# Optimization experiments

Measured on AMD Instinct MI355X. Metric: run time of the kernel, lower is better.

## Reference

```python
import jax, jax.numpy as jnp
import numpy as np

H, W = 32, 32
DIM = 768
NUM_BLOCKS = 4
BLOCK = DIM // NUM_BLOCKS
SCALE = 0.02


def setup_inputs() -> dict:
    key = jax.random.key(0)
    k0, k1, k2, k3, k4 = jax.random.split(key, 5)
    B, N, C = 64, H * W, DIM
    x = jax.random.normal(k0, (B, N, C), dtype=jnp.float32)
    w1 = SCALE * jax.random.normal(k1, (2, NUM_BLOCKS, BLOCK, BLOCK), dtype=jnp.float32)
    b1 = SCALE * jax.random.normal(k2, (2, NUM_BLOCKS, BLOCK), dtype=jnp.float32)
    w2 = SCALE * jax.random.normal(k3, (2, NUM_BLOCKS, BLOCK, BLOCK), dtype=jnp.float32)
    b2 = SCALE * jax.random.normal(k4, (2, NUM_BLOCKS, BLOCK), dtype=jnp.float32)
    return {"x": x, "w1": w1, "b1": b1, "w2": w2, "b2": b2}


def _mul(inp, weights):
    # inp: [B, H, Wf, blocks, d], weights: [blocks, d, k]
    return jnp.einsum('...bd,bdk->...bk', inp, weights)


def reference(x, w1, b1, w2, b2):
    B, N, C = x.shape
    xg = x.reshape(B, H, W, C)
    xf = jnp.fft.rfft2(xg, axes=(1, 2), norm='ortho')  # [B, H, W//2+1, C] complex64
    xf = xf.reshape(B, xf.shape[1], xf.shape[2], NUM_BLOCKS, BLOCK)
    xr, xi = xf.real, xf.imag
    # layer 1: complex block-diagonal linear + ReLU
    r1 = jax.nn.relu(_mul(xr, w1[0]) - _mul(xi, w1[1]) + b1[0])
    i1 = jax.nn.relu(_mul(xr, w1[1]) + _mul(xi, w1[0]) + b1[1])
    # layer 2 (faithful to original: imag uses the already-updated real part)
    r2 = _mul(r1, w2[0]) - _mul(i1, w2[1]) + b2[0]
    i2 = _mul(r2, w2[1]) + _mul(i1, w2[0]) + b2[1]
    xc = (r2 + 1j * i2).reshape(B, r2.shape[1], r2.shape[2], C)
    out = jnp.fft.irfft2(xc, s=(H, W), axes=(1, 2), norm='ortho')
    return out.reshape(B, N, C) + jnp.zeros_like(x)  # bias is zeros (self.bias is None)
```

## Files before the change

kernel.cpp:

```cpp
#include <hip/hip_runtime.h>
#include <cstddef>
#include <cstdint>


typedef __attribute__((ext_vector_type(8))) short bf16x8;
typedef __attribute__((ext_vector_type(4))) float f32x4;

namespace {

constexpr int BATCH = 64;
constexpr int WF    = 17;
constexpr int CC    = 768;
constexpr int BLK   = 192;

constexpr size_t W_ELEMS  = 24u * 36864u;
constexpr size_t TW_ELEMS = 8u * 1024u;
constexpr size_t PW_ELEMS = W_ELEMS + TW_ELEMS;

constexpr int PLANE_U = 48 * 512;

constexpr float C32[32] = {
   1.0000000000f,  0.9807852804f,  0.9238795325f,  0.8314696123f,
   0.7071067812f,  0.5555702330f,  0.3826834324f,  0.1950903220f,
   0.0000000000f, -0.1950903220f, -0.3826834324f, -0.5555702330f,
  -0.7071067812f, -0.8314696123f, -0.9238795325f, -0.9807852804f,
  -1.0000000000f, -0.9807852804f, -0.9238795325f, -0.8314696123f,
  -0.7071067812f, -0.5555702330f, -0.3826834324f, -0.1950903220f,
   0.0000000000f,  0.1950903220f,  0.3826834324f,  0.5555702330f,
   0.7071067812f,  0.8314696123f,  0.9238795325f,  0.9807852804f
};
constexpr float S32[32] = {
   0.0000000000f,  0.1950903220f,  0.3826834324f,  0.5555702330f,
   0.7071067812f,  0.8314696123f,  0.9238795325f,  0.9807852804f,
   1.0000000000f,  0.9807852804f,  0.9238795325f,  0.8314696123f,
   0.7071067812f,  0.5555702330f,  0.3826834324f,  0.1950903220f,
   0.0000000000f, -0.1950903220f, -0.3826834324f, -0.5555702330f,
  -0.7071067812f, -0.8314696123f, -0.9238795325f, -0.9807852804f,
  -1.0000000000f, -0.9807852804f, -0.9238795325f, -0.8314696123f,
  -0.7071067812f, -0.5555702330f, -0.3826834324f, -0.1950903220f
};

}

__device__ __forceinline__ ushort f2bf(float f) {
    union { float f; unsigned u; } v; v.f = f;
    const unsigned r = (v.u + 0x7FFFu + ((v.u >> 16) & 1u)) >> 16;
    return (ushort)r;
}
__device__ __forceinline__ uint pk(float lo, float hi) {
    return (uint)f2bf(lo) | ((uint)f2bf(hi) << 16);
}

__global__ __launch_bounds__(256) void k_pack(const float* __restrict__ w1,
                                              const float* __restrict__ w2,
                                              ushort* __restrict__ pw) {
    const unsigned idx = blockIdx.x * 256u + threadIdx.x;
    if (idx < W_ELEMS) {
        const unsigned mi = idx / 36864u;
        const unsigned r  = idx % 36864u;
        const unsigned kk = r / 6144u;
        const unsigned r2 = r % 6144u;
        const unsigned nf = r2 / 512u;
        const unsigned r3 = r2 % 512u;
        const unsigned lane = r3 / 8u;
        const unsigned i  = r3 % 8u;
        const unsigned d   = kk * 32u + (lane >> 4) * 8u + i;
        const unsigned col = nf * 16u + (lane & 15u);
        const unsigned mat = mi >> 2, blk = mi & 3u;
        const float* src; float sgn = 1.f;
        if      (mat == 0u) src = w1 + (size_t)(0 * 4 + blk) * BLK * BLK;
        else if (mat == 1u) src = w1 + (size_t)(1 * 4 + blk) * BLK * BLK;
        else if (mat == 2u) { src = w1 + (size_t)(1 * 4 + blk) * BLK * BLK; sgn = -1.f; }
        else if (mat == 3u) src = w2 + (size_t)(0 * 4 + blk) * BLK * BLK;
        else if (mat == 4u) src = w2 + (size_t)(1 * 4 + blk) * BLK * BLK;
        else                { src = w2 + (size_t)(1 * 4 + blk) * BLK * BLK; sgn = -1.f; }
        pw[idx] = f2bf(sgn * src[(size_t)d * BLK + col]);
    } else if (idx < PW_ELEMS) {
        const unsigned t = idx - (unsigned)W_ELEMS;
        const unsigned mat = t >> 10;
        const unsigned rr  = t & 1023u;
        const unsigned mf  = rr >> 9;
        const unsigned q   = rr & 511u;
        const unsigned lane = q >> 3, i = q & 7u;
        const unsigned row = mf * 16u + (lane & 15u);
        const unsigned col = (lane >> 4) * 8u + i;
        const unsigned ang = (row * col) & 31u;
        float v;
        if      (mat == 0u) v = C32[ang] * 0.03125f;
        else if (mat == 1u) v = S32[ang] * 0.03125f;
        else if (mat == 2u) v = -S32[ang] * 0.03125f;
        else if (mat == 3u) v = C32[ang];
        else if (mat == 4u) v = S32[ang];
        else if (mat == 5u) v = -S32[ang];
        else if (mat == 6u) {
            if      (col == 0u)  v = 0.03125f;
            else if (col < 16u)  v = 2.f * C32[ang] * 0.03125f;
            else if (col == 16u) v = C32[(16u * row) & 31u] * 0.03125f;
            else                 v = 0.f;
        } else {
            v = (col >= 1u && col <= 15u) ? (-2.f * S32[ang] * 0.03125f) : 0.f;
        }
        pw[idx] = f2bf(v);
    }
}

__global__ __launch_bounds__(256) void k_rfft_w(const float* __restrict__ x,
                                                ushort* __restrict__ spec,
                                                const ushort* __restrict__ pw) {
    __shared__ uint xb[16 * 384];

    const int bid = blockIdx.x;
    const int cq = bid & 3;
    const int hp = (bid >> 2) & 15;
    const int b  = bid >> 6;
    const int tid = threadIdx.x;
    const int wv = tid >> 6, l = tid & 63, lc = l & 15, lg = l >> 4;

#pragma unroll
    for (int it = 0; it < 6; ++it) {
        const int flat = it * 256 + tid;
        const int h  = flat / 768;
        const int rm = flat % 768;
        const int wp = rm / 48;
        const int c4 = rm % 48;
        const float* p = x + ((size_t)(b * 1024 + (hp * 2 + h) * 32 + wp * 2) * CC)
                           + cq * 192 + c4 * 4;
        const float4 a  = *(const float4*)p;
        const float4 bb = *(const float4*)(p + CC);
        uint4 u;
        u.x = pk(a.x, bb.x); u.y = pk(a.y, bb.y);
        u.z = pk(a.z, bb.z); u.w = pk(a.w, bb.w);
        const int col = (h * 192 + c4 * 4) ^ (((wp >> 2) & 3) << 3);
        *(uint4*)&xb[wp * 384 + col] = u;
    }
    __syncthreads();

    const ushort* TW = pw + W_ELEMS;
    bf16x8 ac[2], as[2];
#pragma unroll
    for (int m = 0; m < 2; ++m) {
        ac[m] = *(const bf16x8*)(TW + ((size_t)(3 * 2 + m) * 64 + l) * 8);
        as[m] = *(const bf16x8*)(TW + ((size_t)(5 * 2 + m) * 64 + l) * 8);
    }

    f32x4 aR[2][6] = {}, aI[2][6] = {};
#pragma unroll
    for (int j = 0; j < 6; ++j) {
        const int nf = (j < 3) ? (wv * 3 + j) : (12 + wv * 3 + (j - 3));
        union { bf16x8 v; uint d[4]; } u;
#pragma unroll
        for (int t = 0; t < 4; ++t) {
            const int wp = lg * 4 + t;
            u.d[t] = xb[wp * 384 + ((nf * 16 + lc) ^ (lg << 3))];
        }
#pragma unroll
        for (int m = 0; m < 2; ++m) {
            aR[m][j] = __builtin_amdgcn_mfma_f32_16x16x32_bf16(ac[m], u.v, aR[m][j], 0, 0, 0);
            aI[m][j] = __builtin_amdgcn_mfma_f32_16x16x32_bf16(as[m], u.v, aI[m][j], 0, 0, 0);
        }
    }

    uint* spec32 = (uint*)spec;
    const int swz = (hp & 7) << 1;
#pragma unroll
    for (int m = 0; m < 2; ++m)
#pragma unroll
        for (int j = 0; j < 3; ++j)
#pragma unroll
            for (int r = 0; r < 4; ++r) {
                if (m == 1 && (lg != 0 || r != 0)) continue;
                const int kw = m * 16 + lg * 4 + r;
                const int csub = cq * 12 + wv * 3 + j;
                const size_t pos = ((size_t)(b * WF + kw) * 2) * 12288
                                 + csub * 256 + hp * 16 + (lc ^ swz);
                spec32[pos]         = pk(aR[m][j][r], aR[m][j + 3][r]);
                spec32[pos + 12288] = pk(aI[m][j][r], aI[m][j + 3][r]);
            }
}

__global__ __launch_bounds__(256, 3) void k_fft_mix(
        ushort* __restrict__ spec,
        const ushort* __restrict__ pw,
        const float* __restrict__ b1, const float* __restrict__ b2) {

    __shared__ ushort lds[4][6336];

    const int bid = blockIdx.x;
    const int blk = bid / (BATCH * WF);
    const int rem = bid % (BATCH * WF);
    const int b   = rem / WF;
    const int kw  = rem % WF;
    const int tid = threadIdx.x;
    const int wv = tid >> 6, l = tid & 63, lc = l & 15, lg = l >> 4;

    const size_t gR = ((size_t)(b * WF + kw) * 2) * PLANE_U + blk * 6144;
    const size_t gI = gR + PLANE_U;

#pragma unroll
    for (int j = 0; j < 3; ++j) {
        const int q = tid + 256 * j;
        const int dst = (q >> 6) * 528 + (q & 63) * 8;
        *(uint4*)&lds[0][dst] = *(const uint4*)(spec + gR + q * 8);
        *(uint4*)&lds[1][dst] = *(const uint4*)(spec + gI + q * 8);
    }
    __syncthreads();

    const ushort* TW = pw + W_ELEMS;
    const int col0 = wv * 48;

    {
        bf16x8 xr[3], xi[3];
#pragma unroll
        for (int n = 0; n < 3; ++n) {
            const int csub = wv * 3 + n;
            union { bf16x8 v; uint d[4]; } ur, ui;
#pragma unroll
            for (int t = 0; t < 4; ++t) {
                const int hp = lg * 4 + t;
                const int pos = csub * 528 + hp * 32 + ((lc ^ ((hp & 7) << 1)) << 1);
                ur.d[t] = *(const uint*)&lds[0][pos];
                ui.d[t] = *(const uint*)&lds[1][pos];
            }
            xr[n] = ur.v; xi[n] = ui.v;
        }
        bf16x8 cf[2], sf[2], sfn[2];
#pragma unroll
        for (int m = 0; m < 2; ++m) {
            cf[m]  = *(const bf16x8*)(TW + ((size_t)(0 * 2 + m) * 64 + l) * 8);
            sf[m]  = *(const bf16x8*)(TW + ((size_t)(1 * 2 + m) * 64 + l) * 8);
            sfn[m] = *(const bf16x8*)(TW + ((size_t)(2 * 2 + m) * 64 + l) * 8);
        }
        f32x4 yr[2][3] = {}, yi[2][3] = {};
#pragma unroll
        for (int m = 0; m < 2; ++m)
#pragma unroll
            for (int n = 0; n < 3; ++n) {
                yr[m][n] = __builtin_amdgcn_mfma_f32_16x16x32_bf16(cf[m],  xr[n], yr[m][n], 0, 0, 0);
                yr[m][n] = __builtin_amdgcn_mfma_f32_16x16x32_bf16(sf[m],  xi[n], yr[m][n], 0, 0, 0);
                yi[m][n] = __builtin_amdgcn_mfma_f32_16x16x32_bf16(cf[m],  xi[n], yi[m][n], 0, 0, 0);
                yi[m][n] = __builtin_amdgcn_mfma_f32_16x16x32_bf16(sfn[m], xr[n], yi[m][n], 0, 0, 0);
            }
#pragma unroll
        for (int m = 0; m < 2; ++m)
#pragma unroll
            for (int n = 0; n < 3; ++n)
#pragma unroll
                for (int rp = 0; rp < 2; ++rp) {
                    const uint ur = pk(yr[m][n][2 * rp], yr[m][n][2 * rp + 1]);
                    const uint ui = pk(yi[m][n][2 * rp], yi[m][n][2 * rp + 1]);
                    const int p0 = (wv * 3 + n) * 528 + (m * 16 + lg * 4 + 2 * rp) * 16 + lc;
                    lds[0][p0] = (ushort)ur; lds[0][p0 + 16] = (ushort)(ur >> 16);
                    lds[1][p0] = (ushort)ui; lds[1][p0 + 16] = (ushort)(ui >> 16);
                }
    }
    __syncthreads();

    const ushort* pW1r  = pw + (size_t)(0 * 4 + blk) * 36864;
    const ushort* pW1i  = pw + (size_t)(1 * 4 + blk) * 36864;
    const ushort* pW1in = pw + (size_t)(2 * 4 + blk) * 36864;
    const ushort* pW2r  = pw + (size_t)(3 * 4 + blk) * 36864;
    const ushort* pW2i  = pw + (size_t)(4 * 4 + blk) * 36864;
    const ushort* pW2in = pw + (size_t)(5 * 4 + blk) * 36864;

    {
        f32x4 aR[2][3], aI[2][3];
#pragma unroll
        for (int n = 0; n < 3; ++n) {
            const float br = b1[(size_t)(0 * 4 + blk) * BLK + col0 + n * 16 + lc];
            const float bi = b1[(size_t)(1 * 4 + blk) * BLK + col0 + n * 16 + lc];
#pragma unroll
            for (int m = 0; m < 2; ++m) {
                aR[m][n] = (f32x4){br, br, br, br};
                aI[m][n] = (f32x4){bi, bi, bi, bi};
            }
        }
#pragma unroll
        for (int kk = 0; kk < 6; ++kk) {
            const int csubA = 2 * kk + (lg >> 1);
            const int apos  = csubA * 528 + lc * 16 + (lg & 1) * 8;
            bf16x8 ar[2], ai[2];
#pragma unroll
            for (int m = 0; m < 2; ++m) {
                ar[m] = *(const bf16x8*)&lds[0][apos + m * 256];
                ai[m] = *(const bf16x8*)&lds[1][apos + m * 256];
            }
            bf16x8 wr[3], wi[3], wn[3];
#pragma unroll
            for (int n = 0; n < 3; ++n) {
                const size_t off = ((size_t)(kk * 12 + wv * 3 + n) * 64 + l) * 8;
                wr[n] = *(const bf16x8*)(pW1r + off);
                wi[n] = *(const bf16x8*)(pW1i + off);
                wn[n] = *(const bf16x8*)(pW1in + off);
            }
#pragma unroll
            for (int m = 0; m < 2; ++m)
#pragma unroll
                for (int n = 0; n < 3; ++n) {
                    aR[m][n] = __builtin_amdgcn_mfma_f32_16x16x32_bf16(ar[m], wr[n], aR[m][n], 0, 0, 0);
                    aR[m][n] = __builtin_amdgcn_mfma_f32_16x16x32_bf16(ai[m], wn[n], aR[m][n], 0, 0, 0);
                    aI[m][n] = __builtin_amdgcn_mfma_f32_16x16x32_bf16(ar[m], wi[n], aI[m][n], 0, 0, 0);
                    aI[m][n] = __builtin_amdgcn_mfma_f32_16x16x32_bf16(ai[m], wr[n], aI[m][n], 0, 0, 0);
                }
        }
        __syncthreads();
#pragma unroll
        for (int m = 0; m < 2; ++m)
#pragma unroll
            for (int n = 0; n < 3; ++n)
#pragma unroll
                for (int rp = 0; rp < 2; ++rp) {
                    const uint ur = pk(fmaxf(aR[m][n][2 * rp], 0.f), fmaxf(aR[m][n][2 * rp + 1], 0.f));
                    const uint ui = pk(fmaxf(aI[m][n][2 * rp], 0.f), fmaxf(aI[m][n][2 * rp + 1], 0.f));
                    const int p0 = (wv * 3 + n) * 528 + (m * 16 + lg * 4 + 2 * rp) * 16 + lc;
                    lds[2][p0] = (ushort)ur; lds[2][p0 + 16] = (ushort)(ur >> 16);
                    lds[3][p0] = (ushort)ui; lds[3][p0 + 16] = (ushort)(ui >> 16);
                }
    }
    __syncthreads();

    {
        f32x4 cR[2][3];
#pragma unroll
        for (int n = 0; n < 3; ++n) {
            const float br = b2[(size_t)(0 * 4 + blk) * BLK + col0 + n * 16 + lc];
#pragma unroll
            for (int m = 0; m < 2; ++m) cR[m][n] = (f32x4){br, br, br, br};
        }
#pragma unroll
        for (int kk = 0; kk < 6; ++kk) {
            const int csubA = 2 * kk + (lg >> 1);
            const int apos  = csubA * 528 + lc * 16 + (lg & 1) * 8;
            bf16x8 ar[2], ii[2];
#pragma unroll
            for (int m = 0; m < 2; ++m) {
                ar[m] = *(const bf16x8*)&lds[2][apos + m * 256];
                ii[m] = *(const bf16x8*)&lds[3][apos + m * 256];
            }
            bf16x8 wr[3], wn[3];
#pragma unroll
            for (int n = 0; n < 3; ++n) {
                const size_t off = ((size_t)(kk * 12 + wv * 3 + n) * 64 + l) * 8;
                wr[n] = *(const bf16x8*)(pW2r + off);
                wn[n] = *(const bf16x8*)(pW2in + off);
            }
#pragma unroll
            for (int m = 0; m < 2; ++m)
#pragma unroll
                for (int n = 0; n < 3; ++n) {
                    cR[m][n] = __builtin_amdgcn_mfma_f32_16x16x32_bf16(ar[m], wr[n], cR[m][n], 0, 0, 0);
                    cR[m][n] = __builtin_amdgcn_mfma_f32_16x16x32_bf16(ii[m], wn[n], cR[m][n], 0, 0, 0);
                }
        }
#pragma unroll
        for (int m = 0; m < 2; ++m)
#pragma unroll
            for (int n = 0; n < 3; ++n) {
                const int csub = wv * 3 + n;
#pragma unroll
                for (int rp = 0; rp < 2; ++rp) {
                    const uint p = pk(cR[m][n][2 * rp], cR[m][n][2 * rp + 1]);
                    const int kh0 = m * 16 + lg * 4 + 2 * rp;
                    lds[0][csub * 528 + kh0 * 16 + lc]       = (ushort)p;
                    lds[0][csub * 528 + (kh0 + 1) * 16 + lc] = (ushort)(p >> 16);
                    const int hp = kh0 >> 1;
                    const int post = csub * 528 + hp * 32 + ((lc ^ ((hp & 7) << 1)) << 1);
                    *(uint*)&lds[1][post] = p;
                }
            }
    }
    __syncthreads();

    {
        f32x4 cI[2][3];
#pragma unroll
        for (int n = 0; n < 3; ++n) {
            const float bi = b2[(size_t)(1 * 4 + blk) * BLK + col0 + n * 16 + lc];
#pragma unroll
            for (int m = 0; m < 2; ++m) cI[m][n] = (f32x4){bi, bi, bi, bi};
        }
#pragma unroll
        for (int kk = 0; kk < 6; ++kk) {
            const int csubA = 2 * kk + (lg >> 1);
            const int apos  = csubA * 528 + lc * 16 + (lg & 1) * 8;
            bf16x8 a2[2], i1[2];
#pragma unroll
            for (int m = 0; m < 2; ++m) {
                a2[m] = *(const bf16x8*)&lds[0][apos + m * 256];
                i1[m] = *(const bf16x8*)&lds[3][apos + m * 256];
            }
            bf16x8 wi[3], wr[3];
#pragma unroll
            for (int n = 0; n < 3; ++n) {
                const size_t off = ((size_t)(kk * 12 + wv * 3 + n) * 64 + l) * 8;
                wi[n] = *(const bf16x8*)(pW2i + off);
                wr[n] = *(const bf16x8*)(pW2r + off);
            }
#pragma unroll
            for (int m = 0; m < 2; ++m)
#pragma unroll
                for (int n = 0; n < 3; ++n) {
                    cI[m][n] = __builtin_amdgcn_mfma_f32_16x16x32_bf16(a2[m], wi[n], cI[m][n], 0, 0, 0);
                    cI[m][n] = __builtin_amdgcn_mfma_f32_16x16x32_bf16(i1[m], wr[n], cI[m][n], 0, 0, 0);
                }
        }
#pragma unroll
        for (int m = 0; m < 2; ++m)
#pragma unroll
            for (int n = 0; n < 3; ++n) {
                const int csub = wv * 3 + n;
#pragma unroll
                for (int rp = 0; rp < 2; ++rp) {
                    const int hp = (m * 16 + lg * 4 + 2 * rp) >> 1;
                    const int post = csub * 528 + hp * 32 + ((lc ^ ((hp & 7) << 1)) << 1);
                    *(uint*)&lds[2][post] = pk(cI[m][n][2 * rp], cI[m][n][2 * rp + 1]);
                }
            }
    }

    {
        bf16x8 ci[2], si[2], sn[2];
#pragma unroll
        for (int m = 0; m < 2; ++m) {
            ci[m] = *(const bf16x8*)(TW + ((size_t)(3 * 2 + m) * 64 + l) * 8);
            si[m] = *(const bf16x8*)(TW + ((size_t)(4 * 2 + m) * 64 + l) * 8);
            sn[m] = *(const bf16x8*)(TW + ((size_t)(5 * 2 + m) * 64 + l) * 8);
        }
        bf16x8 r2b[3], i2b[3];
#pragma unroll
        for (int n = 0; n < 3; ++n) {
            const int csub = wv * 3 + n;
            union { bf16x8 v; uint d[4]; } ur, ui;
#pragma unroll
            for (int t = 0; t < 4; ++t) {
                const int hp = lg * 4 + t;
                const int pos = csub * 528 + hp * 32 + ((lc ^ ((hp & 7) << 1)) << 1);
                ur.d[t] = *(const uint*)&lds[1][pos];
                ui.d[t] = *(const uint*)&lds[2][pos];
            }
            r2b[n] = ur.v; i2b[n] = ui.v;
        }
        f32x4 zr[2][3] = {}, zi[2][3] = {};
#pragma unroll
        for (int m = 0; m < 2; ++m)
#pragma unroll
            for (int n = 0; n < 3; ++n) {
                zr[m][n] = __builtin_amdgcn_mfma_f32_16x16x32_bf16(ci[m], r2b[n], zr[m][n], 0, 0, 0);
                zr[m][n] = __builtin_amdgcn_mfma_f32_16x16x32_bf16(sn[m], i2b[n], zr[m][n], 0, 0, 0);
                zi[m][n] = __builtin_amdgcn_mfma_f32_16x16x32_bf16(ci[m], i2b[n], zi[m][n], 0, 0, 0);
                zi[m][n] = __builtin_amdgcn_mfma_f32_16x16x32_bf16(si[m], r2b[n], zi[m][n], 0, 0, 0);
            }
#pragma unroll
        for (int m = 0; m < 2; ++m)
#pragma unroll
            for (int n = 0; n < 3; ++n) {
                const size_t cbase = gR + (size_t)(wv * 3 + n) * 512;
#pragma unroll
                for (int rp = 0; rp < 2; ++rp) {
                    const int hp = (m * 16 + lg * 4 + 2 * rp) >> 1;
                    const size_t pos = cbase + hp * 32 + ((lc ^ ((hp & 7) << 1)) << 1);
                    *(uint*)(spec + pos)           = pk(zr[m][n][2 * rp], zr[m][n][2 * rp + 1]);
                    *(uint*)(spec + pos + PLANE_U) = pk(zi[m][n][2 * rp], zi[m][n][2 * rp + 1]);
                }
            }
    }
}

__global__ __launch_bounds__(256) void k_irfft_w(const ushort* __restrict__ spec,
                                                 float* __restrict__ out,
                                                 const ushort* __restrict__ pw) {
    __shared__ uint rawR[17 * 198];
    __shared__ uint rawI[17 * 198];

    const int bid = blockIdx.x;
    const int cq = bid & 3;
    const int hp = (bid >> 2) & 15;
    const int b  = bid >> 6;
    const int tid = threadIdx.x;
    const int wv = tid >> 6, l = tid & 63, lc = l & 15, lg = l >> 4;

    const uint* spec32 = (const uint*)spec;

#pragma unroll
    for (int it = 0; it < 13; ++it) {
        const int slot = it * 256 + tid;
        if (slot < 3264) {
            const int part = slot & 7;
            const int c2   = slot >> 3;
            const int plane = c2 / 204;
            const int q  = c2 % 204;
            const int kw = q / 12, csub = q % 12;
            const size_t gpos = ((size_t)(b * WF + kw) * 2 + plane) * 12288
                              + (cq * 12 + csub) * 256 + hp * 16 + part * 2;
            const uint2 v = *(const uint2*)(spec32 + gpos);
            uint* dst = plane ? rawI : rawR;
            *(uint2*)&dst[kw * 198 + csub * 16 + part * 2] = v;
        }
    }
    __syncthreads();

    const ushort* TW = pw + W_ELEMS;
    bf16x8 twA[2], twB[2];
#pragma unroll
    for (int m = 0; m < 2; ++m) {
        twA[m] = *(const bf16x8*)(TW + ((size_t)(6 * 2 + m) * 64 + l) * 8);
        twB[m] = *(const bf16x8*)(TW + ((size_t)(7 * 2 + m) * 64 + l) * 8);
    }

    int rowoff[8];
#pragma unroll
    for (int i = 0; i < 8; ++i) {
        int kwv = lg * 8 + i;
        if (kwv > 16) kwv = 16;
        rowoff[i] = kwv * 396;
    }

    const ushort* rr = (const ushort*)rawR;
    const ushort* ri = (const ushort*)rawI;
    const int swz = (hp & 7) << 1;

    f32x4 acc[2][6] = {};
#pragma unroll
    for (int j = 0; j < 6; ++j) {
        const int coll = (wv * 6 + j) * 16 + lc;
        const int h  = coll & 1;
        const int cL = coll >> 1;
        const int bu = ((cL >> 4) * 16 + ((cL & 15) ^ swz)) * 2 + h;
        union { bf16x8 v; ushort s[8]; } fr, fi;
#pragma unroll
        for (int i = 0; i < 8; ++i) {
            fr.s[i] = rr[rowoff[i] + bu];
            fi.s[i] = ri[rowoff[i] + bu];
        }
#pragma unroll
        for (int m = 0; m < 2; ++m) {
            acc[m][j] = __builtin_amdgcn_mfma_f32_16x16x32_bf16(twA[m], fr.v, acc[m][j], 0, 0, 0);
            acc[m][j] = __builtin_amdgcn_mfma_f32_16x16x32_bf16(twB[m], fi.v, acc[m][j], 0, 0, 0);
        }
    }

#pragma unroll
    for (int m = 0; m < 2; ++m)
#pragma unroll
        for (int j = 0; j < 6; ++j) {
            const int coll = (wv * 6 + j) * 16 + lc;
            const int h  = coll & 1;
            const int c  = cq * 192 + (coll >> 1);
#pragma unroll
            for (int r = 0; r < 4; ++r) {
                const int w = m * 16 + lg * 4 + r;
                out[((size_t)(b * 1024 + (hp * 2 + h) * 32 + w)) * CC + c] = acc[m][j][r];
            }
        }
}

extern "C" void kernel_launch(void* const* d_in, const int* in_sizes, int n_in,
                              void* d_out, int out_size, void* d_ws, size_t ws_size,
                              hipStream_t stream) {
    const float* x  = (const float*)d_in[0];
    const float* w1 = (const float*)d_in[1];
    const float* b1 = (const float*)d_in[2];
    const float* w2 = (const float*)d_in[3];
    const float* b2 = (const float*)d_in[4];
    float* out = (float*)d_out;

    ushort* pw   = (ushort*)d_ws;
    ushort* spec = pw + PW_ELEMS;

    k_pack<<<dim3((unsigned)(PW_ELEMS / 256)), dim3(256), 0, stream>>>(w1, w2, pw);
    k_rfft_w<<<dim3(BATCH * 16 * 4), dim3(256), 0, stream>>>(x, spec, pw);
    k_fft_mix<<<dim3(4 * BATCH * WF), dim3(256), 0, stream>>>(spec, pw, b1, b2);
    k_irfft_w<<<dim3(BATCH * 16 * 4), dim3(256), 0, stream>>>(spec, out, pw);
}
```

Before: 263.8 us.

## Negate activations in registers and cut LDS buffers to raise occupancy

Drops the pre-negated weight copies (W1i and W2i negated) and instead flips the bf16 sign bits of the activation fragments in registers before the MFMA. This removes one global weight-fragment load stream per layer and shrinks the packed weight buffer. It also reuses LDS planes so the kernel needs three 6336-element buffers instead of four, and raises launch_bounds min blocks from 3 to 4. Two extra __syncthreads are added to protect the buffer reuse, which adds some synchronisation cost.

```diff
diff --git a/kernel.cpp b/kernel.cpp
--- a/kernel.cpp
+++ b/kernel.cpp
@@ -13,7 +13,7 @@
 constexpr int CC    = 768;
 constexpr int BLK   = 192;
 
-constexpr size_t W_ELEMS  = 24u * 36864u;
+constexpr size_t W_ELEMS  = 16u * 36864u;
 constexpr size_t TW_ELEMS = 8u * 1024u;
 constexpr size_t PW_ELEMS = W_ELEMS + TW_ELEMS;
 
@@ -50,6 +50,12 @@
 __device__ __forceinline__ uint pk(float lo, float hi) {
     return (uint)f2bf(lo) | ((uint)f2bf(hi) << 16);
 }
+__device__ __forceinline__ bf16x8 neg8(bf16x8 a) {
+    union { bf16x8 v; uint4 u; } t; t.v = a;
+    t.u.x ^= 0x80008000u; t.u.y ^= 0x80008000u;
+    t.u.z ^= 0x80008000u; t.u.w ^= 0x80008000u;
+    return t.v;
+}
 
 __global__ __launch_bounds__(256) void k_pack(const float* __restrict__ w1,
                                               const float* __restrict__ w2,
@@ -67,14 +73,12 @@
         const unsigned d   = kk * 32u + (lane >> 4) * 8u + i;
         const unsigned col = nf * 16u + (lane & 15u);
         const unsigned mat = mi >> 2, blk = mi & 3u;
-        const float* src; float sgn = 1.f;
+        const float* src;
         if      (mat == 0u) src = w1 + (size_t)(0 * 4 + blk) * BLK * BLK;
         else if (mat == 1u) src = w1 + (size_t)(1 * 4 + blk) * BLK * BLK;
-        else if (mat == 2u) { src = w1 + (size_t)(1 * 4 + blk) * BLK * BLK; sgn = -1.f; }
-        else if (mat == 3u) src = w2 + (size_t)(0 * 4 + blk) * BLK * BLK;
-        else if (mat == 4u) src = w2 + (size_t)(1 * 4 + blk) * BLK * BLK;
-        else                { src = w2 + (size_t)(1 * 4 + blk) * BLK * BLK; sgn = -1.f; }
-        pw[idx] = f2bf(sgn * src[(size_t)d * BLK + col]);
+        else if (mat == 2u) src = w2 + (size_t)(0 * 4 + blk) * BLK * BLK;
+        else                src = w2 + (size_t)(1 * 4 + blk) * BLK * BLK;
+        pw[idx] = f2bf(src[(size_t)d * BLK + col]);
     } else if (idx < PW_ELEMS) {
         const unsigned t = idx - (unsigned)W_ELEMS;
         const unsigned mat = t >> 10;
@@ -178,12 +182,12 @@
             }
 }
 
-__global__ __launch_bounds__(256, 3) void k_fft_mix(
+__global__ __launch_bounds__(256, 4) void k_fft_mix(
         ushort* __restrict__ spec,
         const ushort* __restrict__ pw,
         const float* __restrict__ b1, const float* __restrict__ b2) {
 
-    __shared__ ushort lds[4][6336];
+    __shared__ ushort lds[3][6336];
 
     const int bid = blockIdx.x;
     const int blk = bid / (BATCH * WF);
@@ -255,12 +259,10 @@
     }
     __syncthreads();
 
-    const ushort* pW1r  = pw + (size_t)(0 * 4 + blk) * 36864;
-    const ushort* pW1i  = pw + (size_t)(1 * 4 + blk) * 36864;
-    const ushort* pW1in = pw + (size_t)(2 * 4 + blk) * 36864;
-    const ushort* pW2r  = pw + (size_t)(3 * 4 + blk) * 36864;
-    const ushort* pW2i  = pw + (size_t)(4 * 4 + blk) * 36864;
-    const ushort* pW2in = pw + (size_t)(5 * 4 + blk) * 36864;
+    const ushort* pW1r = pw + (size_t)(0 * 4 + blk) * 36864;
+    const ushort* pW1i = pw + (size_t)(1 * 4 + blk) * 36864;
+    const ushort* pW2r = pw + (size_t)(2 * 4 + blk) * 36864;
+    const ushort* pW2i = pw + (size_t)(3 * 4 + blk) * 36864;
 
     {
         f32x4 aR[2][3], aI[2][3];
@@ -278,28 +280,28 @@
         for (int kk = 0; kk < 6; ++kk) {
             const int csubA = 2 * kk + (lg >> 1);
             const int apos  = csubA * 528 + lc * 16 + (lg & 1) * 8;
-            bf16x8 ar[2], ai[2];
+            bf16x8 ar[2], ai[2], ain[2];
 #pragma unroll
             for (int m = 0; m < 2; ++m) {
-                ar[m] = *(const bf16x8*)&lds[0][apos + m * 256];
-                ai[m] = *(const bf16x8*)&lds[1][apos + m * 256];
-            }
-            bf16x8 wr[3], wi[3], wn[3];
+                ar[m]  = *(const bf16x8*)&lds[0][apos + m * 256];
+                ai[m]  = *(const bf16x8*)&lds[1][apos + m * 256];
+                ain[m] = neg8(ai[m]);
+            }
+            bf16x8 wr[3], wi[3];
 #pragma unroll
             for (int n = 0; n < 3; ++n) {
                 const size_t off = ((size_t)(kk * 12 + wv * 3 + n) * 64 + l) * 8;
                 wr[n] = *(const bf16x8*)(pW1r + off);
                 wi[n] = *(const bf16x8*)(pW1i + off);
-                wn[n] = *(const bf16x8*)(pW1in + off);
             }
 #pragma unroll
             for (int m = 0; m < 2; ++m)
 #pragma unroll
                 for (int n = 0; n < 3; ++n) {
-                    aR[m][n] = __builtin_amdgcn_mfma_f32_16x16x32_bf16(ar[m], wr[n], aR[m][n], 0, 0, 0);
-                    aR[m][n] = __builtin_amdgcn_mfma_f32_16x16x32_bf16(ai[m], wn[n], aR[m][n], 0, 0, 0);
-                    aI[m][n] = __builtin_amdgcn_mfma_f32_16x16x32_bf16(ar[m], wi[n], aI[m][n], 0, 0, 0);
-                    aI[m][n] = __builtin_amdgcn_mfma_f32_16x16x32_bf16(ai[m], wr[n], aI[m][n], 0, 0, 0);
+                    aR[m][n] = __builtin_amdgcn_mfma_f32_16x16x32_bf16(ar[m],  wr[n], aR[m][n], 0, 0, 0);
+                    aR[m][n] = __builtin_amdgcn_mfma_f32_16x16x32_bf16(ain[m], wi[n], aR[m][n], 0, 0, 0);
+                    aI[m][n] = __builtin_amdgcn_mfma_f32_16x16x32_bf16(ar[m],  wi[n], aI[m][n], 0, 0, 0);
+                    aI[m][n] = __builtin_amdgcn_mfma_f32_16x16x32_bf16(ai[m],  wr[n], aI[m][n], 0, 0, 0);
                 }
         }
         __syncthreads();
@@ -312,8 +314,8 @@
                     const uint ur = pk(fmaxf(aR[m][n][2 * rp], 0.f), fmaxf(aR[m][n][2 * rp + 1], 0.f));
                     const uint ui = pk(fmaxf(aI[m][n][2 * rp], 0.f), fmaxf(aI[m][n][2 * rp + 1], 0.f));
                     const int p0 = (wv * 3 + n) * 528 + (m * 16 + lg * 4 + 2 * rp) * 16 + lc;
-                    lds[2][p0] = (ushort)ur; lds[2][p0 + 16] = (ushort)(ur >> 16);
-                    lds[3][p0] = (ushort)ui; lds[3][p0 + 16] = (ushort)(ui >> 16);
+                    lds[0][p0] = (ushort)ur; lds[0][p0 + 16] = (ushort)(ur >> 16);
+                    lds[1][p0] = (ushort)ui; lds[1][p0 + 16] = (ushort)(ui >> 16);
                 }
     }
     __syncthreads();
@@ -330,27 +332,28 @@
         for (int kk = 0; kk < 6; ++kk) {
             const int csubA = 2 * kk + (lg >> 1);
             const int apos  = csubA * 528 + lc * 16 + (lg & 1) * 8;
-            bf16x8 ar[2], ii[2];
+            bf16x8 ar[2], ain[2];
 #pragma unroll
             for (int m = 0; m < 2; ++m) {
-                ar[m] = *(const bf16x8*)&lds[2][apos + m * 256];
-                ii[m] = *(const bf16x8*)&lds[3][apos + m * 256];
-            }
-            bf16x8 wr[3], wn[3];
+                ar[m]  = *(const bf16x8*)&lds[0][apos + m * 256];
+                ain[m] = neg8(*(const bf16x8*)&lds[1][apos + m * 256]);
+            }
+            bf16x8 wr[3], wi[3];
 #pragma unroll
             for (int n = 0; n < 3; ++n) {
                 const size_t off = ((size_t)(kk * 12 + wv * 3 + n) * 64 + l) * 8;
                 wr[n] = *(const bf16x8*)(pW2r + off);
-                wn[n] = *(const bf16x8*)(pW2in + off);
+                wi[n] = *(const bf16x8*)(pW2i + off);
             }
 #pragma unroll
             for (int m = 0; m < 2; ++m)
 #pragma unroll
                 for (int n = 0; n < 3; ++n) {
-                    cR[m][n] = __builtin_amdgcn_mfma_f32_16x16x32_bf16(ar[m], wr[n], cR[m][n], 0, 0, 0);
-                    cR[m][n] = __builtin_amdgcn_mfma_f32_16x16x32_bf16(ii[m], wn[n], cR[m][n], 0, 0, 0);
-                }
-        }
+                    cR[m][n] = __builtin_amdgcn_mfma_f32_16x16x32_bf16(ar[m],  wr[n], cR[m][n], 0, 0, 0);
+                    cR[m][n] = __builtin_amdgcn_mfma_f32_16x16x32_bf16(ain[m], wi[n], cR[m][n], 0, 0, 0);
+                }
+        }
+        __syncthreads();
 #pragma unroll
         for (int m = 0; m < 2; ++m)
 #pragma unroll
@@ -364,7 +367,7 @@
                     lds[0][csub * 528 + (kh0 + 1) * 16 + lc] = (ushort)(p >> 16);
                     const int hp = kh0 >> 1;
                     const int post = csub * 528 + hp * 32 + ((lc ^ ((hp & 7) << 1)) << 1);
-                    *(uint*)&lds[1][post] = p;
+                    *(uint*)&lds[2][post] = p;
                 }
             }
     }
@@ -386,7 +389,7 @@
 #pragma unroll
             for (int m = 0; m < 2; ++m) {
                 a2[m] = *(const bf16x8*)&lds[0][apos + m * 256];
-                i1[m] = *(const bf16x8*)&lds[3][apos + m * 256];
+                i1[m] = *(const bf16x8*)&lds[1][apos + m * 256];
             }
             bf16x8 wi[3], wr[3];
 #pragma unroll
@@ -403,6 +406,7 @@
                     cI[m][n] = __builtin_amdgcn_mfma_f32_16x16x32_bf16(i1[m], wr[n], cI[m][n], 0, 0, 0);
                 }
         }
+        __syncthreads();
 #pragma unroll
         for (int m = 0; m < 2; ++m)
 #pragma unroll
@@ -412,7 +416,7 @@
                 for (int rp = 0; rp < 2; ++rp) {
                     const int hp = (m * 16 + lg * 4 + 2 * rp) >> 1;
                     const int post = csub * 528 + hp * 32 + ((lc ^ ((hp & 7) << 1)) << 1);
-                    *(uint*)&lds[2][post] = pk(cI[m][n][2 * rp], cI[m][n][2 * rp + 1]);
+                    *(uint*)&lds[1][post] = pk(cI[m][n][2 * rp], cI[m][n][2 * rp + 1]);
                 }
             }
     }
@@ -434,8 +438,8 @@
             for (int t = 0; t < 4; ++t) {
                 const int hp = lg * 4 + t;
                 const int pos = csub * 528 + hp * 32 + ((lc ^ ((hp & 7) << 1)) << 1);
-                ur.d[t] = *(const uint*)&lds[1][pos];
-                ui.d[t] = *(const uint*)&lds[2][pos];
+                ur.d[t] = *(const uint*)&lds[2][pos];
+                ui.d[t] = *(const uint*)&lds[1][pos];
             }
             r2b[n] = ur.v; i2b[n] = ui.v;
         }
```

New measurement: 285.5 us. 1.08x slower.
